# Kernel tuning notes

Measured on AMD Instinct MI355X. Metric: run time of the kernel, lower is better.

The kernel has to match this reference:

```python
import jax, jax.numpy as jnp
import numpy as np
import math

D_MODEL = 1024
HEADS = 16
D_K = D_MODEL // HEADS
B, S = 4, 2048


def setup_inputs() -> dict:
    key = jax.random.key(0)
    ks = jax.random.split(key, 7)
    scale = 1.0 / math.sqrt(D_MODEL)
    inp = {
        "q": jax.random.normal(ks[0], (B, S, D_MODEL), dtype=jnp.float32),
        "k": jax.random.normal(ks[1], (B, S, D_MODEL), dtype=jnp.float32),
        "v": jax.random.normal(ks[2], (B, S, D_MODEL), dtype=jnp.float32),
        # Linear(d_model, d_model, bias=False) weights, stored [out, in] torch-style
        "W_q": jax.random.normal(ks[3], (D_MODEL, D_MODEL), dtype=jnp.float32) * scale,
        "W_k": jax.random.normal(ks[4], (D_MODEL, D_MODEL), dtype=jnp.float32) * scale,
        "W_v": jax.random.normal(ks[5], (D_MODEL, D_MODEL), dtype=jnp.float32) * scale,
        "W_o": jax.random.normal(ks[6], (D_MODEL, D_MODEL), dtype=jnp.float32) * scale,
    }
    return inp


def reference(q, k, v, W_q, W_k, W_v, W_o):
    # projections (torch Linear: x @ W.T)
    query = jnp.einsum("bsd,ed->bse", q, W_q)
    key_ = jnp.einsum("bsd,ed->bse", k, W_k)
    value = jnp.einsum("bsd,ed->bse", v, W_v)
    # split heads -> [B, H, S, d_k]
    def split(x):
        return x.reshape(B, S, HEADS, D_K).transpose(0, 2, 1, 3)
    Q, K, V = split(query), split(key_), split(value)
    # scaled dot-product attention, full [B,H,S,S] scores (naive, faithful)
    scores = jnp.einsum("bhqd,bhkd->bhqk", Q, K) / math.sqrt(D_K)
    attn = jax.nn.softmax(scores, axis=-1)
    x = jnp.einsum("bhqk,bhkd->bhqd", attn, V)
    x = x.transpose(0, 2, 1, 3).reshape(B, S, D_MODEL)
    return jnp.einsum("bsd,ed->bse", x, W_o)
```

## Files before the change

### kernel.cpp

```cpp
#include <hip/hip_runtime.h>
#include <stdint.h>

#define NHEAD 16
#define DKH 64
#define BBATCH 4
#define SEQ 2048
#define MROWS (BBATCH*SEQ)
#define DMODEL 1024

typedef __attribute__((ext_vector_type(8))) __bf16 bf16x8;
typedef __attribute__((ext_vector_type(4))) float f32x4;

__device__ __forceinline__ unsigned short f2bf(float x) {
  unsigned int u = __float_as_uint(x);
  u += 0x7FFFu + ((u >> 16) & 1u);
  return (unsigned short)(u >> 16);
}
__device__ __forceinline__ unsigned int pkbf(float a, float b) {
  return __builtin_amdgcn_perm(__float_as_uint(b) + 0x8000u,
                               __float_as_uint(a) + 0x8000u, 0x07060302u);
}
__device__ __forceinline__ unsigned int pkbf_t(float a, float b) {
  return __builtin_amdgcn_perm(__float_as_uint(b), __float_as_uint(a), 0x07060302u);
}
__device__ __forceinline__ void gl_lds16(const void* g, void* l) {
  __builtin_amdgcn_global_load_lds(
      (const __attribute__((address_space(1))) unsigned int*)g,
      (__attribute__((address_space(3))) unsigned int*)l, 16, 0, 0);
}
__device__ __forceinline__ f32x4 mfma16(bf16x8 a, bf16x8 b, f32x4 c) {
  return __builtin_amdgcn_mfma_f32_16x16x32_bf16(a, b, c, 0, 0, 0);
}

__global__ __launch_bounds__(256) void cvt_all(
    const float* __restrict__ s0, const float* __restrict__ s1,
    const float* __restrict__ s2, const float* __restrict__ s3,
    const float* __restrict__ s4, const float* __restrict__ s5,
    const float* __restrict__ s6,
    unsigned short* __restrict__ d0, unsigned short* __restrict__ d1,
    unsigned short* __restrict__ d2, unsigned short* __restrict__ d3,
    unsigned short* __restrict__ d4, unsigned short* __restrict__ d5,
    unsigned short* __restrict__ d6) {
  const int NB = 2097152;
  const int NW = 262144;
  int i = blockIdx.x * 256 + threadIdx.x;
  const float* src; unsigned short* dst; int off;
  if      (i < NB)          { src = s0; dst = d0; off = i; }
  else if (i < 2*NB)        { src = s1; dst = d1; off = i - NB; }
  else if (i < 3*NB)        { src = s2; dst = d2; off = i - 2*NB; }
  else if (i < 3*NB + NW)   { src = s3; dst = d3; off = i - 3*NB; }
  else if (i < 3*NB + 2*NW) { src = s4; dst = d4; off = i - 3*NB - NW; }
  else if (i < 3*NB + 3*NW) { src = s5; dst = d5; off = i - 3*NB - 2*NW; }
  else                      { src = s6; dst = d6; off = i - 3*NB - 3*NW; }
  float4 x = ((const float4*)src)[off];
  uint2 o; o.x = pkbf(x.x, x.y); o.y = pkbf(x.z, x.w);
  ((uint2*)dst)[off] = o;
}

__global__ __launch_bounds__(256) void proj_gemm(
    const unsigned short* __restrict__ A0, const unsigned short* __restrict__ A1,
    const unsigned short* __restrict__ A2,
    const unsigned short* __restrict__ B0, const unsigned short* __restrict__ B1,
    const unsigned short* __restrict__ B2,
    unsigned short* __restrict__ O0, unsigned short* __restrict__ O1,
    unsigned short* __restrict__ O2) {
  __shared__ __align__(16) unsigned short smem[16384];
  unsigned short* sA = smem;
  unsigned short* sB = smem + 8192;
  const int z = blockIdx.z;
  const unsigned short* Ah = (z == 0) ? A0 : ((z == 1) ? A1 : A2);
  const unsigned short* Bh = (z == 0) ? B0 : ((z == 1) ? B1 : B2);
  unsigned short* outp = (z == 0) ? O0 : ((z == 1) ? O1 : O2);
  const int t = threadIdx.x;
  const int bm = blockIdx.x, bn = blockIdx.y;
  const int lane = t & 63, lm = lane & 15, quad = lane >> 4;
  const int w = t >> 6, wr = w >> 1, wc = w & 1;

  f32x4 acc[4][4];
#pragma unroll
  for (int i = 0; i < 4; ++i)
#pragma unroll
    for (int j = 0; j < 4; ++j) acc[i][j] = (f32x4){0.f, 0.f, 0.f, 0.f};

  for (int kk = 0; kk < 16; ++kk) {
#pragma unroll
    for (int jj = 0; jj < 4; ++jj) {
      int cid = jj * 256 + t;
      int r = cid >> 3, c = cid & 7;
      int gcol = kk * 64 + ((c ^ (r & 7)) * 8);
      gl_lds16(Ah + (bm * 128 + r) * 1024 + gcol, sA + cid * 8);
      gl_lds16(Bh + (bn * 128 + r) * 1024 + gcol, sB + cid * 8);
    }
    __syncthreads();
#pragma unroll
    for (int kc = 0; kc < 2; ++kc) {
      bf16x8 af[4], bf[4];
#pragma unroll
      for (int i = 0; i < 4; ++i) {
        int m = wr * 64 + i * 16 + lm;
        int nn = wc * 64 + i * 16 + lm;
        int slot = ((kc * 4 + quad) ^ (lm & 7)) * 8;
        af[i] = *(const bf16x8*)(sA + m * 64 + slot);
        bf[i] = *(const bf16x8*)(sB + nn * 64 + slot);
      }
#pragma unroll
      for (int i = 0; i < 4; ++i)
#pragma unroll
        for (int j = 0; j < 4; ++j) acc[i][j] = mfma16(af[i], bf[j], acc[i][j]);
    }
    __syncthreads();
  }

  if (z < 2) {
    float scale = (z == 0) ? 0.125f * 1.44269504f : 1.0f;
#pragma unroll
    for (int i = 0; i < 4; ++i)
#pragma unroll
      for (int j = 0; j < 4; ++j)
#pragma unroll
        for (int r = 0; r < 4; ++r) {
          int m = bm * 128 + wr * 64 + i * 16 + quad * 4 + r;
          int nn = bn * 128 + wc * 64 + j * 16 + lm;
          int b = m >> 11, s = m & 2047, h = nn >> 6, d = nn & 63;
          outp[((b * 16 + h) * 2048 + s) * 64 + d] = f2bf(acc[i][j][r] * scale);
        }
  } else {
#pragma unroll
    for (int i = 0; i < 4; ++i)
#pragma unroll
      for (int j = 0; j < 4; ++j)
#pragma unroll
        for (int r = 0; r < 4; ++r) {
          int ml = wr * 64 + i * 16 + quad * 4 + r;
          int nl = wc * 64 + j * 16 + lm;
          smem[nl * 128 + (((ml >> 3) ^ (nl & 15)) << 3) + (ml & 7)] =
              f2bf(acc[i][j][r]);
        }
    __syncthreads();
    int nl = t >> 1, half = t & 1;
    int e = bn * 128 + nl, h = e >> 6, d = e & 63;
    int mg = bm * 128;
    int b = mg >> 11, s0 = mg & 2047;
    uint4* dstp = (uint4*)(outp + ((b * 16 + h) * 64 + d) * 2048 + s0);
#pragma unroll
    for (int u = 0; u < 8; ++u) {
      int c = half * 8 + u;
      int slot = c ^ (nl & 15);
      dstp[c] = *(const uint4*)(smem + nl * 128 + slot * 8);
    }
  }
}

__global__ __launch_bounds__(256, 2) void flash_attn(
    const unsigned short* __restrict__ Qw, const unsigned short* __restrict__ Kw,
    const unsigned short* __restrict__ Vt, unsigned short* __restrict__ Xw) {
  __shared__ __align__(16) unsigned short sK[2][128 * 64];
  __shared__ __align__(16) unsigned short sV[2][64 * 128];
  const int t = threadIdx.x;
  const int bh = (blockIdx.x << 3) | blockIdx.z;
  const int qt = blockIdx.y;
  const int lane = t & 63, lm = lane & 15, quad = lane >> 4;
  const int w = t >> 6;

  const unsigned short* gq = Qw + (long)bh * SEQ * 64 + (long)qt * 256 * 64;
  const unsigned short* gk = Kw + (long)bh * SEQ * 64;
  const unsigned short* gv = Vt + (long)bh * 64 * SEQ;

  bf16x8 qf[4][2];
#pragma unroll
  for (int i = 0; i < 4; ++i)
#pragma unroll
    for (int kc = 0; kc < 2; ++kc)
      qf[i][kc] = *(const bf16x8*)(gq + (w * 64 + i * 16 + lm) * 64 + kc * 32 + quad * 8);

  f32x4 o[4][4];
  f32x4 lacc[4];
#pragma unroll
  for (int i = 0; i < 4; ++i) {
    lacc[i] = (f32x4){0.f, 0.f, 0.f, 0.f};
#pragma unroll
    for (int nv = 0; nv < 4; ++nv) o[i][nv] = (f32x4){0.f, 0.f, 0.f, 0.f};
  }

  auto stage = [&](int kt, int b) {
#pragma unroll
    for (int is = 0; is < 4; ++is) {
      int cid = is * 256 + t;
      int rk = cid >> 3, ck = cid & 7;
      int srk = (rk & 3) | ((rk & 8) >> 1);
      gl_lds16(gk + kt * 128 * 64 + rk * 64 + ((ck ^ srk) * 8), &sK[b][cid * 8]);
      int rv = cid >> 4, cv = cid & 15;
      gl_lds16(gv + kt * 128 + rv * SEQ + ((cv ^ (rv & 15)) * 8), &sV[b][cid * 8]);
    }
  };

  uint4 ou; ou.x = ou.y = ou.z = ou.w = 0x3F803F80u;
  const bf16x8 ones = __builtin_bit_cast(bf16x8, ou);

  stage(0, 0);
  __syncthreads();

  for (int kt = 0; kt < 16; ++kt) {
    const int cur = kt & 1;
    if (kt < 15) stage(kt + 1, cur ^ 1);
    const unsigned short* sk = &sK[cur][0];
    const unsigned short* sv = &sV[cur][0];
#pragma unroll
    for (int p = 0; p < 4; ++p) {
      bf16x8 kf[2][2];
#pragma unroll
      for (int tt = 0; tt < 2; ++tt) {
        int g = p * 32 + 8 * (lm >> 2) + (lm & 3) + 4 * tt;
        int sg = (g & 3) | ((g & 8) >> 1);
        kf[tt][0] = *(const bf16x8*)(sk + g * 64 + ((quad ^ sg) * 8));
        kf[tt][1] = *(const bf16x8*)(sk + g * 64 + (((4 + quad) ^ sg) * 8));
      }
      bf16x8 pfrag[4];
#pragma unroll
      for (int i = 0; i < 4; ++i) {
        f32x4 s0 = (f32x4){0.f, 0.f, 0.f, 0.f};
        f32x4 s1 = (f32x4){0.f, 0.f, 0.f, 0.f};
        __builtin_amdgcn_s_setprio(1);
        s0 = mfma16(kf[0][0], qf[i][0], s0);
        s0 = mfma16(kf[0][1], qf[i][1], s0);
        s1 = mfma16(kf[1][0], qf[i][0], s1);
        s1 = mfma16(kf[1][1], qf[i][1], s1);
        __builtin_amdgcn_s_setprio(0);
        float p0[4], p1[4];
#pragma unroll
        for (int r = 0; r < 4; ++r) {
          p0[r] = __builtin_amdgcn_exp2f(s0[r]);
          p1[r] = __builtin_amdgcn_exp2f(s1[r]);
        }
        uint4 pw;
        pw.x = pkbf_t(p0[0], p0[1]); pw.y = pkbf_t(p0[2], p0[3]);
        pw.z = pkbf_t(p1[0], p1[1]); pw.w = pkbf_t(p1[2], p1[3]);
        pfrag[i] = __builtin_bit_cast(bf16x8, pw);
      }
      __builtin_amdgcn_s_setprio(1);
#pragma unroll
      for (int i = 0; i < 4; ++i) lacc[i] = mfma16(pfrag[i], ones, lacc[i]);
#pragma unroll
      for (int nv = 0; nv < 4; ++nv) {
        bf16x8 vb = *(const bf16x8*)(sv + (nv * 16 + lm) * 128 + (((p * 4 + quad) ^ lm) * 8));
#pragma unroll
        for (int i = 0; i < 4; ++i) o[i][nv] = mfma16(pfrag[i], vb, o[i][nv]);
      }
      __builtin_amdgcn_s_setprio(0);
    }
    __syncthreads();
  }

  int b = bh >> 4, h = bh & 15;
#pragma unroll
  for (int i = 0; i < 4; ++i) {
    float inv[4];
#pragma unroll
    for (int r = 0; r < 4; ++r) inv[r] = __builtin_amdgcn_rcpf(lacc[i][r]);
#pragma unroll
    for (int nv = 0; nv < 4; ++nv)
#pragma unroll
      for (int r = 0; r < 4; ++r) {
        int q = qt * 256 + w * 64 + i * 16 + quad * 4 + r;
        int d = nv * 16 + lm;
        Xw[((long)(b * 2048 + q) * 16 + h) * 64 + d] = f2bf(o[i][nv][r] * inv[r]);
      }
  }
}

__global__ __launch_bounds__(256) void out_gemm(
    const unsigned short* __restrict__ A, const unsigned short* __restrict__ Bw,
    float* __restrict__ C) {
  __shared__ __align__(16) unsigned short smem[16384];
  unsigned short* sA = smem;
  unsigned short* sB = smem + 8192;
  const int t = threadIdx.x;
  const int bm = blockIdx.x, bn = blockIdx.y;
  const int lane = t & 63, lm = lane & 15, quad = lane >> 4;
  const int w = t >> 6, wr = w >> 1, wc = w & 1;

  f32x4 acc[4][4];
#pragma unroll
  for (int i = 0; i < 4; ++i)
#pragma unroll
    for (int j = 0; j < 4; ++j) acc[i][j] = (f32x4){0.f, 0.f, 0.f, 0.f};

  for (int kk = 0; kk < 16; ++kk) {
#pragma unroll
    for (int jj = 0; jj < 4; ++jj) {
      int cid = jj * 256 + t;
      int r = cid >> 3, c = cid & 7;
      int gcol = kk * 64 + ((c ^ (r & 7)) * 8);
      gl_lds16(A + (bm * 128 + r) * 1024 + gcol, sA + cid * 8);
      gl_lds16(Bw + (bn * 128 + r) * 1024 + gcol, sB + cid * 8);
    }
    __syncthreads();
#pragma unroll
    for (int kc = 0; kc < 2; ++kc) {
      bf16x8 af[4], bf[4];
#pragma unroll
      for (int i = 0; i < 4; ++i) {
        int m = wr * 64 + i * 16 + lm;
        int nn = wc * 64 + i * 16 + lm;
        int slot = ((kc * 4 + quad) ^ (lm & 7)) * 8;
        af[i] = *(const bf16x8*)(sA + m * 64 + slot);
        bf[i] = *(const bf16x8*)(sB + nn * 64 + slot);
      }
#pragma unroll
      for (int i = 0; i < 4; ++i)
#pragma unroll
        for (int j = 0; j < 4; ++j) acc[i][j] = mfma16(af[i], bf[j], acc[i][j]);
    }
    __syncthreads();
  }
#pragma unroll
  for (int i = 0; i < 4; ++i)
#pragma unroll
    for (int j = 0; j < 4; ++j)
#pragma unroll
      for (int r = 0; r < 4; ++r) {
        int m = bm * 128 + wr * 64 + i * 16 + quad * 4 + r;
        int nn = bn * 128 + wc * 64 + j * 16 + lm;
        C[m * 1024 + nn] = acc[i][j][r];
      }
}

extern "C" void kernel_launch(void* const* d_in, const int* in_sizes, int n_in,
                              void* d_out, int out_size, void* d_ws, size_t ws_size,
                              hipStream_t stream) {
  const float* q  = (const float*)d_in[0];
  const float* k  = (const float*)d_in[1];
  const float* v  = (const float*)d_in[2];
  const float* Wq = (const float*)d_in[3];
  const float* Wk = (const float*)d_in[4];
  const float* Wv = (const float*)d_in[5];
  const float* Wo = (const float*)d_in[6];

  char* ws = (char*)d_ws;
  const size_t MK = (size_t)MROWS * DMODEL;
  const size_t KK = (size_t)DMODEL * DMODEL;
  size_t off = 0;
  auto nxt = [&](size_t elems) { unsigned short* p = (unsigned short*)(ws + off); off += elems * 2; return p; };
  unsigned short* q_b  = nxt(MK);
  unsigned short* k_b  = nxt(MK);
  unsigned short* v_b  = nxt(MK);
  unsigned short* Wq_b = nxt(KK);
  unsigned short* Wk_b = nxt(KK);
  unsigned short* Wv_b = nxt(KK);
  unsigned short* Wo_b = nxt(KK);
  unsigned short* Qw = nxt(MK);
  unsigned short* Kw = nxt(MK);
  unsigned short* Vt = nxt(MK);
  unsigned short* Xw = nxt(MK);
  (void)ws_size; (void)in_sizes; (void)n_in; (void)out_size;

  cvt_all<<<28672, 256, 0, stream>>>(q, k, v, Wq, Wk, Wv, Wo,
                                     q_b, k_b, v_b, Wq_b, Wk_b, Wv_b, Wo_b);
  proj_gemm<<<dim3(64, 8, 3), 256, 0, stream>>>(q_b, k_b, v_b,
                                                Wq_b, Wk_b, Wv_b,
                                                Qw, Kw, Vt);
  flash_attn<<<dim3(8, 8, 8), 256, 0, stream>>>(Qw, Kw, Vt, Xw);
  out_gemm<<<dim3(64, 8), 256, 0, stream>>>(Xw, Wo_b, (float*)d_out);
}
```

Before: 312.3 us.

## Double-buffer LDS tiles in projection and output GEMMs to overlap loads

```diff
diff --git a/kernel.cpp b/kernel.cpp
--- a/kernel.cpp
+++ b/kernel.cpp
@@ -57,16 +57,14 @@
   ((uint2*)dst)[off] = o;
 }
 
-__global__ __launch_bounds__(256) void proj_gemm(
+__global__ __launch_bounds__(256, 2) void proj_gemm(
     const unsigned short* __restrict__ A0, const unsigned short* __restrict__ A1,
     const unsigned short* __restrict__ A2,
     const unsigned short* __restrict__ B0, const unsigned short* __restrict__ B1,
     const unsigned short* __restrict__ B2,
     unsigned short* __restrict__ O0, unsigned short* __restrict__ O1,
     unsigned short* __restrict__ O2) {
-  __shared__ __align__(16) unsigned short smem[16384];
-  unsigned short* sA = smem;
-  unsigned short* sB = smem + 8192;
+  __shared__ __align__(16) unsigned short smem[2][16384];
   const int z = blockIdx.z;
   const unsigned short* Ah = (z == 0) ? A0 : ((z == 1) ? A1 : A2);
   const unsigned short* Bh = (z == 0) ? B0 : ((z == 1) ? B1 : B2);
@@ -82,16 +80,25 @@
 #pragma unroll
     for (int j = 0; j < 4; ++j) acc[i][j] = (f32x4){0.f, 0.f, 0.f, 0.f};
 
-  for (int kk = 0; kk < 16; ++kk) {
+  auto stage = [&](int kk, int b) {
 #pragma unroll
     for (int jj = 0; jj < 4; ++jj) {
       int cid = jj * 256 + t;
       int r = cid >> 3, c = cid & 7;
       int gcol = kk * 64 + ((c ^ (r & 7)) * 8);
-      gl_lds16(Ah + (bm * 128 + r) * 1024 + gcol, sA + cid * 8);
-      gl_lds16(Bh + (bn * 128 + r) * 1024 + gcol, sB + cid * 8);
-    }
-    __syncthreads();
+      gl_lds16(Ah + (bm * 128 + r) * 1024 + gcol, &smem[b][cid * 8]);
+      gl_lds16(Bh + (bn * 128 + r) * 1024 + gcol, &smem[b][8192 + cid * 8]);
+    }
+  };
+
+  stage(0, 0);
+  __syncthreads();
+
+  for (int kk = 0; kk < 16; ++kk) {
+    const int cur = kk & 1;
+    if (kk < 15) stage(kk + 1, cur ^ 1);
+    const unsigned short* sA = &smem[cur][0];
+    const unsigned short* sB = &smem[cur][8192];
 #pragma unroll
     for (int kc = 0; kc < 2; ++kc) {
       bf16x8 af[4], bf[4];
@@ -125,6 +132,7 @@
           outp[((b * 16 + h) * 2048 + s) * 64 + d] = f2bf(acc[i][j][r] * scale);
         }
   } else {
+    unsigned short* scr = &smem[0][0];
 #pragma unroll
     for (int i = 0; i < 4; ++i)
 #pragma unroll
@@ -133,7 +141,7 @@
         for (int r = 0; r < 4; ++r) {
           int ml = wr * 64 + i * 16 + quad * 4 + r;
           int nl = wc * 64 + j * 16 + lm;
-          smem[nl * 128 + (((ml >> 3) ^ (nl & 15)) << 3) + (ml & 7)] =
+          scr[nl * 128 + (((ml >> 3) ^ (nl & 15)) << 3) + (ml & 7)] =
               f2bf(acc[i][j][r]);
         }
     __syncthreads();
@@ -146,7 +154,7 @@
     for (int u = 0; u < 8; ++u) {
       int c = half * 8 + u;
       int slot = c ^ (nl & 15);
-      dstp[c] = *(const uint4*)(smem + nl * 128 + slot * 8);
+      dstp[c] = *(const uint4*)(scr + nl * 128 + slot * 8);
     }
   }
 }
@@ -268,12 +276,10 @@
   }
 }
 
-__global__ __launch_bounds__(256) void out_gemm(
+__global__ __launch_bounds__(256, 2) void out_gemm(
     const unsigned short* __restrict__ A, const unsigned short* __restrict__ Bw,
     float* __restrict__ C) {
-  __shared__ __align__(16) unsigned short smem[16384];
-  unsigned short* sA = smem;
-  unsigned short* sB = smem + 8192;
+  __shared__ __align__(16) unsigned short smem[2][16384];
   const int t = threadIdx.x;
   const int bm = blockIdx.x, bn = blockIdx.y;
   const int lane = t & 63, lm = lane & 15, quad = lane >> 4;
@@ -285,16 +291,25 @@
 #pragma unroll
     for (int j = 0; j < 4; ++j) acc[i][j] = (f32x4){0.f, 0.f, 0.f, 0.f};
 
-  for (int kk = 0; kk < 16; ++kk) {
+  auto stage = [&](int kk, int b) {
 #pragma unroll
     for (int jj = 0; jj < 4; ++jj) {
       int cid = jj * 256 + t;
       int r = cid >> 3, c = cid & 7;
       int gcol = kk * 64 + ((c ^ (r & 7)) * 8);
-      gl_lds16(A + (bm * 128 + r) * 1024 + gcol, sA + cid * 8);
-      gl_lds16(Bw + (bn * 128 + r) * 1024 + gcol, sB + cid * 8);
-    }
-    __syncthreads();
+      gl_lds16(A + (bm * 128 + r) * 1024 + gcol, &smem[b][cid * 8]);
+      gl_lds16(Bw + (bn * 128 + r) * 1024 + gcol, &smem[b][8192 + cid * 8]);
+    }
+  };
+
+  stage(0, 0);
+  __syncthreads();
+
+  for (int kk = 0; kk < 16; ++kk) {
+    const int cur = kk & 1;
+    if (kk < 15) stage(kk + 1, cur ^ 1);
+    const unsigned short* sA = &smem[cur][0];
+    const unsigned short* sB = &smem[cur][8192];
 #pragma unroll
     for (int kc = 0; kc < 2; ++kc) {
       bf16x8 af[4], bf[4];
```

Result: faster. 297.6 us (-4.7%).
